# Kernel tuning notes

Measured on AMD Instinct MI355X. Metric: run time of the kernel, lower is better.

The kernel has to match this reference:

```python
import jax, jax.numpy as jnp
import numpy as np

NUM_TREES = 100
TREE_DEPTH = 5
INPUT_DIM = 256
NUM_CLASSES = 64
BATCH = 8192
NUM_NODES = 2 ** TREE_DEPTH - 1   # 31 decision nodes per tree
NUM_LEAVES = 2 ** TREE_DEPTH      # 32 leaves per tree


def setup_inputs() -> dict:
    key = jax.random.key(0)
    k_x, k_w, k_b, k_l = jax.random.split(key, 4)
    x = jax.random.normal(k_x, (BATCH, INPUT_DIM), dtype=jnp.float32)
    # stacked per-tree decision-node params (torch.randn init)
    node_w = jax.random.normal(k_w, (NUM_TREES, NUM_NODES, INPUT_DIM), dtype=jnp.float32)
    node_b = jax.random.normal(k_b, (NUM_TREES, NUM_NODES), dtype=jnp.float32)
    leaves = jax.random.normal(k_l, (NUM_TREES, NUM_LEAVES, NUM_CLASSES), dtype=jnp.float32)
    return {"x": x, "node_w": node_w, "node_b": node_b, "leaves": leaves}


def reference(x, node_w, node_b, leaves):
    # x: [B, D]; node_w: [T, Nn, D]; node_b: [T, Nn]; leaves: [T, Nl, C]
    T = node_w.shape[0]
    B = x.shape[0]
    depth = int(np.log2(leaves.shape[1]))
    idx = jnp.zeros((T, B), dtype=jnp.int32)
    for _ in range(depth):  # small fixed depth loop
        # gather each sample's routing node per tree: [T, B, D] and [T, B]
        w_g = jnp.take_along_axis(node_w, idx[:, :, None], axis=1)
        b_g = jnp.take_along_axis(node_b, idx, axis=1)
        decisions = jax.nn.sigmoid(jnp.einsum('tbd,bd->tb', w_g, x) + b_g)
        idx = 2 * idx + (decisions <= 0.5).astype(jnp.int32)
    # leaf gather: [T, B, C], then forest average over trees -> [B, C]
    tree_preds = jnp.take_along_axis(leaves, idx[:, :, None], axis=1)
    return jnp.mean(tree_preds, axis=0)
```

## Files before the change

### kernel.cpp

```cpp
#include <hip/hip_runtime.h>


typedef __bf16 bf16;
typedef __attribute__((ext_vector_type(8))) __bf16 bf16x8;
typedef __attribute__((ext_vector_type(4))) float f32x4;

#define NTREES 100
#define NB     8192
#define ND     256
#define NNODES 31
#define NLEAF  32
#define NCLS   64
#define TAU    2.0e-3f

static __device__ __forceinline__ void gload16(const void* g, void* l) {
    __builtin_amdgcn_global_load_lds(
        (const __attribute__((address_space(1))) void*)g,
        (__attribute__((address_space(3))) void*)l, 16, 0, 0);
}

static __device__ __forceinline__ int traverse(const float z[16], float* mn_out) {
    float a0 = z[0];
    bool d0 = a0 <= 0.f;
    float a1 = d0 ? z[1] : z[0];
    bool d1 = a1 <= 0.f;
    float a2 = d0 ? (d1 ? z[3] : z[2]) : (d1 ? z[1] : z[0]);
    bool d2 = a2 <= 0.f;
    float m0 = d2 ? z[1] : z[0], m1 = d2 ? z[3] : z[2];
    float m2 = d2 ? z[5] : z[4], m3 = d2 ? z[7] : z[6];
    float p0 = d1 ? m1 : m0, p1 = d1 ? m3 : m2;
    float a3 = d0 ? p1 : p0;
    bool d3 = a3 <= 0.f;
    float n0 = d3 ? z[1] : z[0],  n1 = d3 ? z[3] : z[2];
    float n2 = d3 ? z[5] : z[4],  n3 = d3 ? z[7] : z[6];
    float n4 = d3 ? z[9] : z[8],  n5 = d3 ? z[11] : z[10];
    float n6 = d3 ? z[13] : z[12], n7 = d3 ? z[15] : z[14];
    float q0 = d2 ? n1 : n0, q1 = d2 ? n3 : n2;
    float q2 = d2 ? n5 : n4, q3 = d2 ? n7 : n6;
    float r0 = d1 ? q1 : q0, r1 = d1 ? q3 : q2;
    float a4 = d0 ? r1 : r0;
    bool d4 = a4 <= 0.f;
    *mn_out = fminf(fminf(fminf(fabsf(a0), fabsf(a1)),
                          fminf(fabsf(a2), fabsf(a3))), fabsf(a4));
    return ((int)d0 << 4) | ((int)d1 << 3) | ((int)d2 << 2)
         | ((int)d3 << 1) | (int)d4;
}

__global__ void prep(const float* __restrict__ x, const float* __restrict__ wf,
                     const float* __restrict__ lv,
                     bf16* __restrict__ xh, bf16* __restrict__ xl,
                     bf16* __restrict__ wimg, bf16* __restrict__ lv16) {
    if (blockIdx.x < 1024) {
        int i = blockIdx.x * 256 + threadIdx.x;
        int m  = i & 15;
        int dq = (i >> 4) & 31;
        int g  = i >> 9;
        const float* src = x + (size_t)(g * 16 + m) * ND + dq * 8;
        bf16x8 h8, l8;
#pragma unroll
        for (int e = 0; e < 8; ++e) {
            float f = src[e];
            bf16 h = (bf16)f;
            h8[e] = h;
            l8[e] = (bf16)(f - (float)h);
        }
        *(bf16x8*)(xh + (size_t)i * 8) = h8;
        *(bf16x8*)(xl + (size_t)i * 8) = l8;
    } else if (blockIdx.x < 1232) {
        int i = (blockIdx.x - 1024) * 256 + threadIdx.x;
        int oct_g = i & 31;
        int row   = (i >> 5) & 127;
        int tg    = i >> 12;
        int tree  = tg * 8 + (row >> 4), node = row & 15;
        bf16x8 h8, l8;
        if (tree < NTREES) {
            const float* src = wf + ((size_t)tree * NNODES + node) * ND + oct_g * 8;
#pragma unroll
            for (int e = 0; e < 8; ++e) {
                float f = src[e];
                bf16 h = (bf16)f;
                h8[e] = h;
                l8[e] = (bf16)(f - (float)h);
            }
        } else {
#pragma unroll
            for (int e = 0; e < 8; ++e) { h8[e] = (bf16)0.f; l8[e] = (bf16)0.f; }
        }
        int kq = oct_g >> 3, oct = oct_g & 7, cp = oct ^ (row & 7);
        size_t b = (size_t)tg * 65536 + (size_t)kq * 16384 + row * 64 + cp * 8;
        *(bf16x8*)(wimg + b)        = h8;
        *(bf16x8*)(wimg + b + 8192) = l8;
    } else {
        int i = (blockIdx.x - 1232) * 256 + threadIdx.x;
        lv16[i] = (bf16)lv[i];
    }
}

__global__ __launch_bounds__(256, 2) void forest_all(
    const bf16* __restrict__ xh, const bf16* __restrict__ xl,
    const bf16* __restrict__ wimg,
    const float* __restrict__ x,
    const float* __restrict__ wf,
    const float* __restrict__ bias,
    unsigned char* __restrict__ idxb)
{
    __shared__ char lds[65536];

    const int tid  = threadIdx.x;
    const int wave = tid >> 6;
    const int lane = tid & 63;
    const int m    = lane & 15;
    const int q    = lane >> 4;

    const int lin  = blockIdx.x + gridDim.x * blockIdx.y;
    const int xcd  = lin & 7;
    const int slot = lin >> 3;
    const int mg   = xcd * 4 + (slot / 13);
    const int tg   = slot % 13;

    f32x4 acc[4][8];
#pragma unroll
    for (int mi = 0; mi < 4; ++mi)
#pragma unroll
        for (int ni = 0; ni < 8; ++ni)
            acc[mi][ni] = (f32x4){0.f, 0.f, 0.f, 0.f};

    size_t abase[4];
#pragma unroll
    for (int mi = 0; mi < 4; ++mi)
        abase[mi] = (size_t)(mg * 16 + wave * 4 + mi) * 4096 + lane * 8;

    const bf16* wsrc = wimg + (size_t)tg * 65536;

#pragma unroll
    for (int j = 0; j < 16; ++j) {
        int idx = j * 256 + tid;
        gload16(wsrc + idx * 8, lds + idx * 16);
    }
    bf16x8 cah[4], cal[4], nah[4], nal[4];
#pragma unroll
    for (int mi = 0; mi < 4; ++mi) {
        cah[mi] = *(const bf16x8*)(xh + abase[mi]);
        cal[mi] = *(const bf16x8*)(xl + abase[mi]);
    }
    __syncthreads();

#pragma unroll 1
    for (int kk = 0; kk < 8; ++kk) {
        if (kk == 4) {
            __syncthreads();
#pragma unroll
            for (int j = 0; j < 16; ++j) {
                int idx = j * 256 + tid;
                gload16(wsrc + 32768 + idx * 8, lds + idx * 16);
            }
            __syncthreads();
        }
        const bf16* bufc = (const bf16*)lds + ((kk >> 1) & 1) * 16384;
        const int kkq = kk & 1;
        if (kk < 7) {
#pragma unroll
            for (int mi = 0; mi < 4; ++mi) {
                nah[mi] = *(const bf16x8*)(xh + abase[mi] + (kk + 1) * 512);
                nal[mi] = *(const bf16x8*)(xl + abase[mi] + (kk + 1) * 512);
            }
        }
#pragma unroll
        for (int ni = 0; ni < 8; ++ni) {
            const int n  = ni * 16 + m;
            const int cp = (kkq * 4 + q) ^ (m & 7);
            bf16x8 bh = *(const bf16x8*)(bufc + n * 64 + cp * 8);
            bf16x8 bl = *(const bf16x8*)(bufc + 8192 + n * 64 + cp * 8);
#pragma unroll
            for (int mi = 0; mi < 4; ++mi)
                acc[mi][ni] = __builtin_amdgcn_mfma_f32_16x16x32_bf16(cal[mi], bh, acc[mi][ni], 0, 0, 0);
#pragma unroll
            for (int mi = 0; mi < 4; ++mi)
                acc[mi][ni] = __builtin_amdgcn_mfma_f32_16x16x32_bf16(cah[mi], bl, acc[mi][ni], 0, 0, 0);
#pragma unroll
            for (int mi = 0; mi < 4; ++mi)
                acc[mi][ni] = __builtin_amdgcn_mfma_f32_16x16x32_bf16(cah[mi], bh, acc[mi][ni], 0, 0, 0);
        }
#pragma unroll
        for (int mi = 0; mi < 4; ++mi) { cah[mi] = nah[mi]; cal[mi] = nal[mi]; }
    }
    __syncthreads();

    float biasv[8];
#pragma unroll
    for (int ni = 0; ni < 8; ++ni) {
        int tree = tg * 8 + ni;
        biasv[ni] = (tree < NTREES) ? bias[(size_t)tree * NNODES + m] : 0.f;
    }

    float* ws_ = (float*)lds + wave * 1280;
    const int sg = mg * 256 + wave * 64 + lane;
    unsigned int pk0 = 0, pk1 = 0;
#pragma unroll
    for (int ni = 0; ni < 8; ++ni) {
#pragma unroll
        for (int mi = 0; mi < 4; ++mi)
#pragma unroll
            for (int r = 0; r < 4; ++r)
                ws_[(mi * 16 + q * 4 + r) * 20 + m] = acc[mi][ni][r] + biasv[ni];
        f32x4 z0 = *(f32x4*)&ws_[lane * 20];
        f32x4 z1 = *(f32x4*)&ws_[lane * 20 + 4];
        f32x4 z2 = *(f32x4*)&ws_[lane * 20 + 8];
        f32x4 z3 = *(f32x4*)&ws_[lane * 20 + 12];
        float z[16] = {z0[0], z0[1], z0[2], z0[3], z1[0], z1[1], z1[2], z1[3],
                       z2[0], z2[1], z2[2], z2[3], z3[0], z3[1], z3[2], z3[3]};
        float mn;
        int leaf = traverse(z, &mn);
        const int tree = tg * 8 + ni;
        if (tree < NTREES && mn < TAU) {
            const float* xr = x + (size_t)sg * ND;
            float zc[16];
#pragma unroll
            for (int nd = 0; nd < 16; ++nd) zc[nd] = z[nd];
#pragma unroll
            for (int nd = 0; nd < 16; ++nd) {
                if (fabsf(z[nd]) < TAU) {
                    const float* wr = wf + ((size_t)tree * NNODES + nd) * ND;
                    double s0 = 0.0, s1 = 0.0;
#pragma unroll 4
                    for (int k2 = 0; k2 < 32; ++k2) {
                        f32x4 xv = *(const f32x4*)(xr + k2 * 8);
                        f32x4 wv = *(const f32x4*)(wr + k2 * 8);
                        f32x4 xu = *(const f32x4*)(xr + k2 * 8 + 4);
                        f32x4 wu = *(const f32x4*)(wr + k2 * 8 + 4);
                        s0 += (double)xv[0] * wv[0] + (double)xv[1] * wv[1]
                            + (double)xv[2] * wv[2] + (double)xv[3] * wv[3];
                        s1 += (double)xu[0] * wu[0] + (double)xu[1] * wu[1]
                            + (double)xu[2] * wu[2] + (double)xu[3] * wu[3];
                    }
                    double zt = s0 + s1 + (double)bias[(size_t)tree * NNODES + nd];
                    zc[nd] = (zt <= 0.0) ? -1.f : 1.f;
                }
            }
            float mn2;
            leaf = traverse(zc, &mn2);
        }
        if (ni < 4) pk0 |= (unsigned)leaf << (8 * ni);
        else        pk1 |= (unsigned)leaf << (8 * (ni - 4));
    }
    unsigned char* dst = idxb + (size_t)sg * NTREES + tg * 8;
    *(unsigned int*)dst = pk0;
    if (tg < 12) *(unsigned int*)(dst + 4) = pk1;
}

__global__ void leaf_gather(const unsigned char* __restrict__ idxb,
                            const bf16* __restrict__ lv16,
                            float* __restrict__ out) {
    const int wave = threadIdx.x >> 6;
    const int lane = threadIdx.x & 63;
    const int s = blockIdx.x * 4 + wave;
    unsigned int rw = 0;
    if (lane < 25) rw = *(const unsigned int*)(idxb + (size_t)s * NTREES + lane * 4);
    float acc = 0.f;
#pragma unroll 10
    for (int t = 0; t < NTREES; ++t) {
        unsigned int wrd = __shfl(rw, t >> 2);
        int li = (wrd >> ((t & 3) * 8)) & 255;
        acc += (float)lv16[((size_t)t * NLEAF + li) * NCLS + lane];
    }
    out[(size_t)s * NCLS + lane] = acc * 0.01f;
}

extern "C" void kernel_launch(void* const* d_in, const int* in_sizes, int n_in,
                              void* d_out, int out_size, void* d_ws, size_t ws_size,
                              hipStream_t stream) {
    const float* x  = (const float*)d_in[0];
    const float* nw = (const float*)d_in[1];
    const float* nb = (const float*)d_in[2];
    const float* lv = (const float*)d_in[3];
    float* out = (float*)d_out;

    char* ws = (char*)d_ws;
    bf16* xh   = (bf16*)(ws + 0);
    bf16* xl   = (bf16*)(ws + 4194304);
    bf16* wimg = (bf16*)(ws + 8388608);
    unsigned char* idxb = (unsigned char*)(ws + 10092544);
    bf16* lv16 = (bf16*)(ws + 10911744);
    if (ws_size < (size_t)11321344) return;

    prep<<<2032, 256, 0, stream>>>(x, nw, lv, xh, xl, wimg, lv16);
    forest_all<<<dim3(13, 32), 256, 0, stream>>>(xh, xl, wimg, x, nw, nb, idxb);
    leaf_gather<<<NB / 4, 256, 0, stream>>>(idxb, lv16, out);
}
```

Measured before the change: 128.0 us.

## Split fused GEMM+traversal into separate GEMM and traversal kernels via global z buffer

```diff
diff --git a/kernel.cpp b/kernel.cpp
--- a/kernel.cpp
+++ b/kernel.cpp
@@ -96,13 +96,11 @@
     }
 }
 
-__global__ __launch_bounds__(256, 2) void forest_all(
+__global__ __launch_bounds__(256, 2) void gemm_z(
     const bf16* __restrict__ xh, const bf16* __restrict__ xl,
     const bf16* __restrict__ wimg,
-    const float* __restrict__ x,
-    const float* __restrict__ wf,
     const float* __restrict__ bias,
-    unsigned char* __restrict__ idxb)
+    float* __restrict__ zbuf)
 {
     __shared__ char lds[65536];
 
@@ -184,7 +182,6 @@
 #pragma unroll
         for (int mi = 0; mi < 4; ++mi) { cah[mi] = nah[mi]; cal[mi] = nal[mi]; }
     }
-    __syncthreads();
 
     float biasv[8];
 #pragma unroll
@@ -192,60 +189,68 @@
         int tree = tg * 8 + ni;
         biasv[ni] = (tree < NTREES) ? bias[(size_t)tree * NNODES + m] : 0.f;
     }
-
-    float* ws_ = (float*)lds + wave * 1280;
-    const int sg = mg * 256 + wave * 64 + lane;
-    unsigned int pk0 = 0, pk1 = 0;
+    const int sbase = mg * 256 + wave * 64;
 #pragma unroll
     for (int ni = 0; ni < 8; ++ni) {
-#pragma unroll
-        for (int mi = 0; mi < 4; ++mi)
-#pragma unroll
-            for (int r = 0; r < 4; ++r)
-                ws_[(mi * 16 + q * 4 + r) * 20 + m] = acc[mi][ni][r] + biasv[ni];
-        f32x4 z0 = *(f32x4*)&ws_[lane * 20];
-        f32x4 z1 = *(f32x4*)&ws_[lane * 20 + 4];
-        f32x4 z2 = *(f32x4*)&ws_[lane * 20 + 8];
-        f32x4 z3 = *(f32x4*)&ws_[lane * 20 + 12];
-        float z[16] = {z0[0], z0[1], z0[2], z0[3], z1[0], z1[1], z1[2], z1[3],
-                       z2[0], z2[1], z2[2], z2[3], z3[0], z3[1], z3[2], z3[3]};
-        float mn;
-        int leaf = traverse(z, &mn);
-        const int tree = tg * 8 + ni;
-        if (tree < NTREES && mn < TAU) {
-            const float* xr = x + (size_t)sg * ND;
-            float zc[16];
-#pragma unroll
-            for (int nd = 0; nd < 16; ++nd) zc[nd] = z[nd];
-#pragma unroll
-            for (int nd = 0; nd < 16; ++nd) {
-                if (fabsf(z[nd]) < TAU) {
-                    const float* wr = wf + ((size_t)tree * NNODES + nd) * ND;
-                    double s0 = 0.0, s1 = 0.0;
+        const int t = tg * 8 + ni;
+        if (t < NTREES) {
+#pragma unroll
+            for (int mi = 0; mi < 4; ++mi)
+#pragma unroll
+                for (int r = 0; r < 4; ++r) {
+                    int s = sbase + mi * 16 + q * 4 + r;
+                    zbuf[((size_t)s * NTREES + t) * 16 + m] = acc[mi][ni][r] + biasv[ni];
+                }
+        }
+    }
+}
+
+__global__ void traverse_k(const float* __restrict__ zbuf,
+                           const float* __restrict__ x,
+                           const float* __restrict__ wf,
+                           const float* __restrict__ bias,
+                           unsigned char* __restrict__ idxb) {
+    const int t = threadIdx.x & 127;
+    const int s = blockIdx.x * 2 + (threadIdx.x >> 7);
+    if (t >= NTREES) return;
+    const float* zr = zbuf + ((size_t)s * NTREES + t) * 16;
+    f32x4 z0 = *(const f32x4*)(zr);
+    f32x4 z1 = *(const f32x4*)(zr + 4);
+    f32x4 z2 = *(const f32x4*)(zr + 8);
+    f32x4 z3 = *(const f32x4*)(zr + 12);
+    float z[16] = {z0[0], z0[1], z0[2], z0[3], z1[0], z1[1], z1[2], z1[3],
+                   z2[0], z2[1], z2[2], z2[3], z3[0], z3[1], z3[2], z3[3]};
+    float mn;
+    int leaf = traverse(z, &mn);
+    if (mn < TAU) {
+        const float* xr = x + (size_t)s * ND;
+        float zc[16];
+#pragma unroll
+        for (int nd = 0; nd < 16; ++nd) zc[nd] = z[nd];
+#pragma unroll
+        for (int nd = 0; nd < 16; ++nd) {
+            if (fabsf(z[nd]) < TAU) {
+                const float* wr = wf + ((size_t)t * NNODES + nd) * ND;
+                double s0 = 0.0, s1 = 0.0;
 #pragma unroll 4
-                    for (int k2 = 0; k2 < 32; ++k2) {
-                        f32x4 xv = *(const f32x4*)(xr + k2 * 8);
-                        f32x4 wv = *(const f32x4*)(wr + k2 * 8);
-                        f32x4 xu = *(const f32x4*)(xr + k2 * 8 + 4);
-                        f32x4 wu = *(const f32x4*)(wr + k2 * 8 + 4);
-                        s0 += (double)xv[0] * wv[0] + (double)xv[1] * wv[1]
-                            + (double)xv[2] * wv[2] + (double)xv[3] * wv[3];
-                        s1 += (double)xu[0] * wu[0] + (double)xu[1] * wu[1]
-                            + (double)xu[2] * wu[2] + (double)xu[3] * wu[3];
-                    }
-                    double zt = s0 + s1 + (double)bias[(size_t)tree * NNODES + nd];
-                    zc[nd] = (zt <= 0.0) ? -1.f : 1.f;
+                for (int k2 = 0; k2 < 32; ++k2) {
+                    f32x4 xv = *(const f32x4*)(xr + k2 * 8);
+                    f32x4 wv = *(const f32x4*)(wr + k2 * 8);
+                    f32x4 xu = *(const f32x4*)(xr + k2 * 8 + 4);
+                    f32x4 wu = *(const f32x4*)(wr + k2 * 8 + 4);
+                    s0 += (double)xv[0] * wv[0] + (double)xv[1] * wv[1]
+                        + (double)xv[2] * wv[2] + (double)xv[3] * wv[3];
+                    s1 += (double)xu[0] * wu[0] + (double)xu[1] * wu[1]
+                        + (double)xu[2] * wu[2] + (double)xu[3] * wu[3];
                 }
-            }
-            float mn2;
-            leaf = traverse(zc, &mn2);
-        }
-        if (ni < 4) pk0 |= (unsigned)leaf << (8 * ni);
-        else        pk1 |= (unsigned)leaf << (8 * (ni - 4));
-    }
-    unsigned char* dst = idxb + (size_t)sg * NTREES + tg * 8;
-    *(unsigned int*)dst = pk0;
-    if (tg < 12) *(unsigned int*)(dst + 4) = pk1;
+                double zt = s0 + s1 + (double)bias[(size_t)t * NNODES + nd];
+                zc[nd] = (zt <= 0.0) ? -1.f : 1.f;
+            }
+        }
+        float mn2;
+        leaf = traverse(zc, &mn2);
+    }
+    idxb[(size_t)s * NTREES + t] = (unsigned char)leaf;
 }
 
 __global__ void leaf_gather(const unsigned char* __restrict__ idxb,
@@ -281,9 +286,11 @@
     bf16* wimg = (bf16*)(ws + 8388608);
     unsigned char* idxb = (unsigned char*)(ws + 10092544);
     bf16* lv16 = (bf16*)(ws + 10911744);
-    if (ws_size < (size_t)11321344) return;
+    float* zbuf = (float*)(ws + 11321344);
+    if (ws_size < (size_t)63750144) return;
 
     prep<<<2032, 256, 0, stream>>>(x, nw, lv, xh, xl, wimg, lv16);
-    forest_all<<<dim3(13, 32), 256, 0, stream>>>(xh, xl, wimg, x, nw, nb, idxb);
+    gemm_z<<<dim3(13, 32), 256, 0, stream>>>(xh, xl, wimg, nb, zbuf);
+    traverse_k<<<NB / 2, 256, 0, stream>>>(zbuf, x, nw, nb, idxb);
     leaf_gather<<<NB / 4, 256, 0, stream>>>(idxb, lv16, out);
 }
```

After: 121.4 us. 5.1% less time.
